# Kernel tuning notes

Hardware: AMD Instinct MI355X
Metric: run time of the kernel (lower is better)

The kernel has to match this reference:

```python
import jax, jax.numpy as jnp
import numpy as np

T = 4096        # tokens
D = 1024        # input_dim
H = 2048        # expert_hidden_dim
O = 1024        # output_dim
E = 8           # num_experts
K = 2           # top_k


def setup_inputs() -> dict:
    key = jax.random.key(0)
    ks = jax.random.split(key, 7)
    s_in = 1.0 / np.sqrt(D)
    s_h = 1.0 / np.sqrt(H)
    return {
        "x": jax.random.normal(ks[0], (T, D), dtype=jnp.float32),
        "Wg": jax.random.uniform(ks[1], (D, E), jnp.float32, -s_in, s_in),
        "bg": jax.random.uniform(ks[2], (E,), jnp.float32, -s_in, s_in),
        "W1": jax.random.uniform(ks[3], (E, D, H), jnp.float32, -s_in, s_in),
        "b1": jax.random.uniform(ks[4], (E, H), jnp.float32, -s_in, s_in),
        "W2": jax.random.uniform(ks[5], (E, H, O), jnp.float32, -s_h, s_h),
        "b2": jax.random.uniform(ks[6], (E, O), jnp.float32, -s_h, s_h),
    }


def reference(x, Wg, bg, W1, b1, W2, b2):
    # Gating: top-k over expert logits, softmax over the k selected logits.
    logits = x @ Wg + bg                                  # [T, E]
    top_vals, top_idx = jax.lax.top_k(logits, K)          # [T, K]
    gates = jax.nn.softmax(top_vals, axis=-1)             # [T, K]

    # Expert MLPs (Linear -> ReLU -> Linear). Each token is processed by the
    # experts it routes to; since an expert's output on x is route-independent,
    # compute all expert outputs once and gather the selected ones (static
    # shapes, jit-friendly equivalent of the masked dispatch loop).
    h = jax.nn.relu(jnp.einsum('td,edh->eth', x, W1) + b1[:, None, :])  # [E,T,H]
    y = jnp.einsum('eth,eho->eto', h, W2) + b2[:, None, :]              # [E,T,O]

    sel = y[top_idx, jnp.arange(T)[:, None]]              # [T, K, O]
    # Weighted combine (scatter_add over batch_idx == per-token sum over K).
    return jnp.sum(sel * gates[..., None], axis=1)        # [T, O]
```

## Files before the change

kernel.cpp:

```cpp
#include <hip/hip_runtime.h>
#include <math.h>


#define T_TOK 4096
#define DIM   1024
#define HID   2048
#define OUTD  1024
#define NE    8

typedef __bf16 bf16_t;
typedef __bf16 bf16x8 __attribute__((ext_vector_type(8)));
typedef float  f32x4  __attribute__((ext_vector_type(4)));

typedef __attribute__((address_space(3))) void       as3_void;
typedef __attribute__((address_space(1))) const void as1_void;
#define GLDS16(src, dst) \
  __builtin_amdgcn_global_load_lds((as1_void*)(src), (as3_void*)(dst), 16, 0, 0)

#define FENCE() asm volatile("" ::: "memory")
#define BARRIER() do { FENCE(); __builtin_amdgcn_s_barrier(); FENCE(); } while (0)

__global__ void k_gate(const float* __restrict__ x, const float* __restrict__ Wg,
                       const float* __restrict__ bg, int* __restrict__ einfo,
                       float2* __restrict__ gpair, bf16_t* __restrict__ xb) {
  int wid  = threadIdx.x >> 6;
  int lane = threadIdx.x & 63;
  int t = blockIdx.x * 4 + wid;

  const float4* xr = (const float4*)(x + (size_t)t * DIM);
  float4 xv4[4];
  float sf[NE];
#pragma unroll
  for (int e = 0; e < NE; ++e) sf[e] = 0.f;

#pragma unroll
  for (int i = 0; i < 4; ++i) {
    int q = lane + 64 * i;
    float4 xv = xr[q];
    xv4[i] = xv;
    int d = q * 4;
#pragma unroll
    for (int c = 0; c < 4; ++c) {
      float xc = (&xv.x)[c];
      const float4* wr = (const float4*)(Wg + (size_t)(d + c) * NE);
      float4 w0 = wr[0], w1 = wr[1];
      sf[0] += xc * w0.x; sf[1] += xc * w0.y;
      sf[2] += xc * w0.z; sf[3] += xc * w0.w;
      sf[4] += xc * w1.x; sf[5] += xc * w1.y;
      sf[6] += xc * w1.z; sf[7] += xc * w1.w;
    }
  }

  ushort4* xbr = (ushort4*)(xb + (size_t)t * DIM);
#pragma unroll
  for (int i = 0; i < 4; ++i) {
    union { bf16_t b[4]; ushort4 u; } cv;
    cv.b[0] = (bf16_t)xv4[i].x; cv.b[1] = (bf16_t)xv4[i].y;
    cv.b[2] = (bf16_t)xv4[i].z; cv.b[3] = (bf16_t)xv4[i].w;
    xbr[lane + 64 * i] = cv.u;
  }

  double s[NE];
#pragma unroll
  for (int e = 0; e < NE; ++e) s[e] = (double)sf[e];
#pragma unroll
  for (int off = 32; off > 0; off >>= 1) {
#pragma unroll
    for (int e = 0; e < NE; ++e) s[e] += __shfl_xor(s[e], off);
  }

  if (lane == 0) {
    double v0 = -1e300, v1 = -1e300;
    int i0 = 0, i1 = 0;
#pragma unroll
    for (int e = 0; e < NE; ++e) {
      double v = s[e] + (double)bg[e];
      if (v > v0)      { v1 = v0; i1 = i0; v0 = v; i0 = e; }
      else if (v > v1) { v1 = v;  i1 = e; }
    }
    float ex = expf((float)(v1 - v0));
    float inv = 1.0f / (1.0f + ex);
    einfo[t] = i0 | (i1 << 8);
    gpair[t] = make_float2(inv, ex * inv);
  }
}

__global__ void k_bin(const int* __restrict__ einfo, const float2* __restrict__ gpair,
                      int* __restrict__ cnt, int* __restrict__ offs,
                      int* __restrict__ elist, float* __restrict__ egate,
                      int* __restrict__ tokrec) {
  __shared__ int scnt[NE];
  int w = threadIdx.x >> 6;
  int lane = threadIdx.x & 63;
  unsigned long long below = (lane == 0) ? 0ull : ((~0ull) >> (64 - lane));
  int base = 0;
  for (int c = 0; c < T_TOK / 64; ++c) {
    int t = c * 64 + lane;
    int ei = einfo[t];
    float2 g = gpair[t];
    int e0 = ei & 0xff, e1 = ei >> 8;
    bool m0 = (e0 == w);
    bool m  = m0 || (e1 == w);
    unsigned long long mask = __ballot(m);
    if (m) {
      int pos = base + (int)__popcll(mask & below);
      elist[w * T_TOK + pos] = t;
      egate[w * T_TOK + pos] = m0 ? g.x : g.y;
      tokrec[2 * t + (m0 ? 0 : 1)] = (w << 16) | pos;
    }
    base += (int)__popcll(mask);
  }
  if (lane == 0) scnt[w] = base;
  __syncthreads();
  if (threadIdx.x == 0) {
    int a = 0;
#pragma unroll
    for (int e = 0; e < NE; ++e) {
      cnt[e] = scnt[e];
      offs[e] = a;
      a += scnt[e];
    }
    offs[NE] = a;
  }
}

__global__ void k_tr(const float* __restrict__ W, bf16_t* __restrict__ Wt,
                     int R, int C) {
  __shared__ float tile[32][33];
  size_t ebase = (size_t)blockIdx.z * R * C;
  int c0 = blockIdx.x * 32, r0 = blockIdx.y * 32;
  int id = threadIdx.x;
  int rc = id >> 5, cc = id & 31;
#pragma unroll
  for (int i = 0; i < 4; ++i)
    tile[rc + i * 8][cc] = W[ebase + (size_t)(r0 + rc + i * 8) * C + c0 + cc];
  __syncthreads();
  int oc = id >> 4, orp = id & 15;
  ushort2* wt2 = (ushort2*)(Wt + ebase);
#pragma unroll
  for (int i = 0; i < 2; ++i) {
    int c = oc + i * 16;
    union { bf16_t b[2]; ushort2 u; } cv;
    cv.b[0] = (bf16_t)tile[orp * 2][c];
    cv.b[1] = (bf16_t)tile[orp * 2 + 1][c];
    wt2[((size_t)(c0 + c) * R + r0 + orp * 2) >> 1] = cv.u;
  }
}

#define STAGE_A(TT, HH) do { \
    char* _d = smem + ((((TT) & 1) * 2 + (HH)) << 14); \
    GLDS16(Abase + offA[HH][0] + (TT) * 128, _d + dstq0 * 16); \
    GLDS16(Abase + offA[HH][1] + (TT) * 128, _d + dstq1 * 16); } while (0)

#define STAGE_B(TT, HH) do { \
    char* _d = smem + 65536 + ((((TT) & 1) * 2 + (HH)) << 14); \
    GLDS16(Bbase + offB[HH][0] + (TT) * 128, _d + dstq0 * 16); \
    GLDS16(Bbase + offB[HH][1] + (TT) * 128, _d + dstq1 * 16); } while (0)

#define PHASE(Q, TT, NTc) do { \
    const char* _a  = smem + ((((TT) & 1) * 2 + ((Q) >> 1)) << 14); \
    const char* _bb = smem + 65536 + ((((TT) & 1) * 2 + ((Q) & 1)) << 14); \
    bf16x8 af[4][2], bfr[2][2]; \
    _Pragma("unroll") for (int i = 0; i < 4; ++i) \
      _Pragma("unroll") for (int kk = 0; kk < 2; ++kk) \
        af[i][kk] = *(const bf16x8*)(_a + rdA[i][kk]); \
    _Pragma("unroll") for (int j = 0; j < 2; ++j) \
      _Pragma("unroll") for (int kk = 0; kk < 2; ++kk) \
        bfr[j][kk] = *(const bf16x8*)(_bb + rdB[j][kk]); \
    if ((Q) == 0)      { if ((TT) + 1 < (NTc)) STAGE_A((TT) + 1, 1); } \
    else if ((Q) == 1) { if ((TT) + 1 < (NTc)) STAGE_B((TT) + 1, 1); } \
    else if ((Q) == 2) { if ((TT) + 2 < (NTc)) STAGE_A((TT) + 2, 0); } \
    else { \
      if ((TT) + 2 < (NTc)) { STAGE_B((TT) + 2, 0); \
        asm volatile("s_waitcnt vmcnt(4)" ::: "memory"); } \
      else { asm volatile("s_waitcnt vmcnt(0)" ::: "memory"); } \
    } \
    BARRIER(); \
    asm volatile("s_waitcnt lgkmcnt(0)" ::: "memory"); \
    __builtin_amdgcn_sched_barrier(0); \
    __builtin_amdgcn_s_setprio(1); \
    _Pragma("unroll") for (int i = 0; i < 4; ++i) \
      _Pragma("unroll") for (int j = 0; j < 2; ++j) \
        _Pragma("unroll") for (int kk = 0; kk < 2; ++kk) \
          acc[((Q) >> 1) * 4 + i][((Q) & 1) * 2 + j] = \
            __builtin_amdgcn_mfma_f32_16x16x32_bf16(af[i][kk], bfr[j][kk], \
                acc[((Q) >> 1) * 4 + i][((Q) & 1) * 2 + j], 0, 0, 0); \
    __builtin_amdgcn_s_setprio(0); \
    BARRIER(); \
  } while (0)

__launch_bounds__(512, 2)
__global__ void k_gemm1(const bf16_t* __restrict__ xb, const bf16_t* __restrict__ W1t,
                        const float* __restrict__ b1, const int* __restrict__ cnt,
                        const int* __restrict__ offs, const int* __restrict__ elist,
                        bf16_t* __restrict__ hbuf) {
  const int e = blockIdx.z;
  const int count = cnt[e];
  const int rt = blockIdx.y;
  if (rt * 256 >= count) return;
  const int nt = blockIdx.x;

  __shared__ __align__(16) char smem[131072];

  const int tid = threadIdx.x, lane = tid & 63, wid = tid >> 6;
  const int wm = wid >> 2, wn = wid & 3;
  const int fr = lane & 15, lh = lane >> 4;

  unsigned offA[2][2], offB[2][2];
  const int dstq0 = tid, dstq1 = 512 + tid;
#pragma unroll
  for (int j = 0; j < 2; ++j) {
    int q = j * 512 + tid;
    int r = q >> 3, sfg = (q & 7) ^ (r & 7);
#pragma unroll
    for (int h = 0; h < 2; ++h) {
      int gr = rt * 256 + h * 128 + r;
      if (gr > count - 1) gr = count - 1;
      int tok = elist[e * T_TOK + gr];
      offA[h][j] = (unsigned)((tok * DIM + sfg * 8) * 2);
      int brow = nt * 256 + h * 128 + r;
      offB[h][j] = (unsigned)(((e * HID + brow) * DIM + sfg * 8) * 2);
    }
  }
  unsigned rdA[4][2], rdB[2][2];
#pragma unroll
  for (int i = 0; i < 4; ++i) {
    int r = wm * 64 + i * 16 + fr;
#pragma unroll
    for (int kk = 0; kk < 2; ++kk)
      rdA[i][kk] = (unsigned)(r * 128 + (((kk * 4 + lh) ^ (r & 7)) * 16));
  }
#pragma unroll
  for (int j = 0; j < 2; ++j) {
    int r = wn * 32 + j * 16 + fr;
#pragma unroll
    for (int kk = 0; kk < 2; ++kk)
      rdB[j][kk] = (unsigned)(r * 128 + (((kk * 4 + lh) ^ (r & 7)) * 16));
  }

  const char* Abase = (const char*)xb;
  const char* Bbase = (const char*)W1t;

  f32x4 acc[8][4];
#pragma unroll
  for (int i = 0; i < 8; ++i)
#pragma unroll
    for (int j = 0; j < 4; ++j) acc[i][j] = (f32x4){0.f, 0.f, 0.f, 0.f};

  const int NT = DIM / 64;
  STAGE_A(0, 0); STAGE_B(0, 0); STAGE_A(0, 1); STAGE_B(0, 1);
  STAGE_A(1, 0); STAGE_B(1, 0);
  asm volatile("s_waitcnt vmcnt(4)" ::: "memory");
  BARRIER();

  for (int t = 0; t < NT; ++t) {
    PHASE(0, t, NT);
    PHASE(1, t, NT);
    PHASE(2, t, NT);
    PHASE(3, t, NT);
  }

  const int hbase = offs[e];
#pragma unroll
  for (int mi = 0; mi < 8; ++mi) {
#pragma unroll
    for (int rr = 0; rr < 4; ++rr) {
      int rowp = rt * 256 + (mi >> 2) * 128 + wm * 64 + (mi & 3) * 16 + lh * 4 + rr;
      if (rowp < count) {
        size_t hrow = (size_t)(hbase + rowp) * HID;
#pragma unroll
        for (int nj = 0; nj < 4; ++nj) {
          int col = nt * 256 + (nj >> 1) * 128 + wn * 32 + (nj & 1) * 16 + fr;
          float v = acc[mi][nj][rr] + b1[e * HID + col];
          hbuf[hrow + col] = (bf16_t)(v > 0.f ? v : 0.f);
        }
      }
    }
  }
}

__launch_bounds__(512, 2)
__global__ void k_gemm2(const bf16_t* __restrict__ hbuf, const bf16_t* __restrict__ W2t,
                        const float* __restrict__ b2, const int* __restrict__ cnt,
                        const int* __restrict__ offs, const float* __restrict__ egate,
                        float* __restrict__ y) {
  const int e = blockIdx.z;
  const int count = cnt[e];
  const int rt = blockIdx.y;
  if (rt * 256 >= count) return;
  const int nt = blockIdx.x;

  __shared__ __align__(16) char smem[131072];

  const int tid = threadIdx.x, lane = tid & 63, wid = tid >> 6;
  const int wm = wid >> 2, wn = wid & 3;
  const int fr = lane & 15, lh = lane >> 4;
  const int hbase = offs[e];

  unsigned offA[2][2], offB[2][2];
  const int dstq0 = tid, dstq1 = 512 + tid;
#pragma unroll
  for (int j = 0; j < 2; ++j) {
    int q = j * 512 + tid;
    int r = q >> 3, sfg = (q & 7) ^ (r & 7);
#pragma unroll
    for (int h = 0; h < 2; ++h) {
      int gr = rt * 256 + h * 128 + r;
      if (gr > count - 1) gr = count - 1;
      offA[h][j] = (unsigned)(((hbase + gr) * HID + sfg * 8) * 2);
      int brow = nt * 256 + h * 128 + r;
      offB[h][j] = (unsigned)(((e * OUTD + brow) * HID + sfg * 8) * 2);
    }
  }
  unsigned rdA[4][2], rdB[2][2];
#pragma unroll
  for (int i = 0; i < 4; ++i) {
    int r = wm * 64 + i * 16 + fr;
#pragma unroll
    for (int kk = 0; kk < 2; ++kk)
      rdA[i][kk] = (unsigned)(r * 128 + (((kk * 4 + lh) ^ (r & 7)) * 16));
  }
#pragma unroll
  for (int j = 0; j < 2; ++j) {
    int r = wn * 32 + j * 16 + fr;
#pragma unroll
    for (int kk = 0; kk < 2; ++kk)
      rdB[j][kk] = (unsigned)(r * 128 + (((kk * 4 + lh) ^ (r & 7)) * 16));
  }

  const char* Abase = (const char*)hbuf;
  const char* Bbase = (const char*)W2t;

  f32x4 acc[8][4];
#pragma unroll
  for (int i = 0; i < 8; ++i)
#pragma unroll
    for (int j = 0; j < 4; ++j) acc[i][j] = (f32x4){0.f, 0.f, 0.f, 0.f};

  const int NT = HID / 64;
  STAGE_A(0, 0); STAGE_B(0, 0); STAGE_A(0, 1); STAGE_B(0, 1);
  STAGE_A(1, 0); STAGE_B(1, 0);
  asm volatile("s_waitcnt vmcnt(4)" ::: "memory");
  BARRIER();

  for (int t = 0; t < NT; ++t) {
    PHASE(0, t, NT);
    PHASE(1, t, NT);
    PHASE(2, t, NT);
    PHASE(3, t, NT);
  }

#pragma unroll
  for (int mi = 0; mi < 8; ++mi) {
#pragma unroll
    for (int rr = 0; rr < 4; ++rr) {
      int rowp = rt * 256 + (mi >> 2) * 128 + wm * 64 + (mi & 3) * 16 + lh * 4 + rr;
      if (rowp < count) {
        float gate = egate[e * T_TOK + rowp];
        size_t yrow = (size_t)(hbase + rowp) * OUTD;
#pragma unroll
        for (int nj = 0; nj < 4; ++nj) {
          int col = nt * 256 + (nj >> 1) * 128 + wn * 32 + (nj & 1) * 16 + fr;
          y[yrow + col] = gate * (acc[mi][nj][rr] + b2[e * OUTD + col]);
        }
      }
    }
  }
}

__global__ void k_combine(const float* __restrict__ y, const int* __restrict__ offs,
                          const int* __restrict__ tokrec, float* __restrict__ out) {
  int t = blockIdx.x;
  int r0 = tokrec[2 * t], r1 = tokrec[2 * t + 1];
  int s0 = offs[r0 >> 16] + (r0 & 0xffff);
  int s1 = offs[r1 >> 16] + (r1 & 0xffff);
  const float4* ya = (const float4*)(y + (size_t)s0 * OUTD);
  const float4* yb = (const float4*)(y + (size_t)s1 * OUTD);
  float4* o = (float4*)(out + (size_t)t * OUTD);
  int i = threadIdx.x;
  float4 a = ya[i], b = yb[i];
  o[i] = make_float4(a.x + b.x, a.y + b.y, a.z + b.z, a.w + b.w);
}

extern "C" void kernel_launch(void* const* d_in, const int* in_sizes, int n_in,
                              void* d_out, int out_size, void* d_ws, size_t ws_size,
                              hipStream_t stream) {
  const float* x  = (const float*)d_in[0];
  const float* Wg = (const float*)d_in[1];
  const float* bg = (const float*)d_in[2];
  const float* W1 = (const float*)d_in[3];
  const float* b1 = (const float*)d_in[4];
  const float* W2 = (const float*)d_in[5];
  const float* b2 = (const float*)d_in[6];
  float* out = (float*)d_out;

  char* ws = (char*)d_ws;
  int*    cnt    = (int*)(ws);
  int*    offs   = (int*)(ws + 1024);
  int*    tokrec = (int*)(ws + 4096);
  int*    einfo  = (int*)(ws + 36864);
  float2* gpair  = (float2*)(ws + 53248);
  int*    elist  = (int*)(ws + 131072);
  float*  egate  = (float*)(ws + 262144);
  bf16_t* W1t    = (bf16_t*)(ws + (1u << 20));
  float*  y      = (float*)(ws + (1u << 20));
  bf16_t* W2t    = (bf16_t*)(ws + (1u << 20) + (32u << 20));
  bf16_t* xb     = (bf16_t*)(ws + (1u << 20) + (64u << 20));
  bf16_t* hbuf   = (bf16_t*)(ws + (1u << 20) + (72u << 20));

  k_gate<<<T_TOK / 4, 256, 0, stream>>>(x, Wg, bg, einfo, gpair, xb);
  k_bin<<<1, 512, 0, stream>>>(einfo, gpair, cnt, offs, elist, egate, tokrec);
  k_tr<<<dim3(HID / 32, DIM / 32, NE), 256, 0, stream>>>(W1, W1t, DIM, HID);
  k_tr<<<dim3(OUTD / 32, HID / 32, NE), 256, 0, stream>>>(W2, W2t, HID, OUTD);

  k_gemm1<<<dim3(HID / 256, 16, NE), 512, 0, stream>>>(
      xb, W1t, b1, cnt, offs, elist, hbuf);
  k_gemm2<<<dim3(OUTD / 256, 16, NE), 512, 0, stream>>>(
      hbuf, W2t, b2, cnt, offs, egate, y);
  k_combine<<<T_TOK, 256, 0, stream>>>(y, offs, tokrec, out);
}
```

Before: 245.7 us.

## Flatten grouped GEMMs over concatenated expert rows with smaller tiles

Both expert GEMMs now use a flat 1D grid over 128-row tiles of the concatenated routed-token rows (8192 rows). A tile that straddles an expert boundary loops over each expert it touches, recomputing the full K loop and writing only the rows in range. This removes the padded per-expert 256-row grid with its early-exit blocks, and shrinks tiles and LDS to raise occupancy. The old deep 4-phase pipeline with s_setprio and explicit vmcnt waits is replaced by a simpler double-buffered loop with a barrier each K step. That may lose latency hiding and adds redundant MFMA work on boundary tiles.

```diff
diff --git a/kernel.cpp b/kernel.cpp
--- a/kernel.cpp
+++ b/kernel.cpp
@@ -16,9 +16,6 @@
 typedef __attribute__((address_space(1))) const void as1_void;
 #define GLDS16(src, dst) \
   __builtin_amdgcn_global_load_lds((as1_void*)(src), (as3_void*)(dst), 16, 0, 0)
-
-#define FENCE() asm volatile("" ::: "memory")
-#define BARRIER() do { FENCE(); __builtin_amdgcn_s_barrier(); FENCE(); } while (0)
 
 __global__ void k_gate(const float* __restrict__ x, const float* __restrict__ Wg,
                        const float* __restrict__ bg, int* __restrict__ einfo,
@@ -147,224 +144,221 @@
   }
 }
 
-#define STAGE_A(TT, HH) do { \
-    char* _d = smem + ((((TT) & 1) * 2 + (HH)) << 14); \
-    GLDS16(Abase + offA[HH][0] + (TT) * 128, _d + dstq0 * 16); \
-    GLDS16(Abase + offA[HH][1] + (TT) * 128, _d + dstq1 * 16); } while (0)
-
-#define STAGE_B(TT, HH) do { \
-    char* _d = smem + 65536 + ((((TT) & 1) * 2 + (HH)) << 14); \
-    GLDS16(Bbase + offB[HH][0] + (TT) * 128, _d + dstq0 * 16); \
-    GLDS16(Bbase + offB[HH][1] + (TT) * 128, _d + dstq1 * 16); } while (0)
-
-#define PHASE(Q, TT, NTc) do { \
-    const char* _a  = smem + ((((TT) & 1) * 2 + ((Q) >> 1)) << 14); \
-    const char* _bb = smem + 65536 + ((((TT) & 1) * 2 + ((Q) & 1)) << 14); \
-    bf16x8 af[4][2], bfr[2][2]; \
-    _Pragma("unroll") for (int i = 0; i < 4; ++i) \
-      _Pragma("unroll") for (int kk = 0; kk < 2; ++kk) \
-        af[i][kk] = *(const bf16x8*)(_a + rdA[i][kk]); \
-    _Pragma("unroll") for (int j = 0; j < 2; ++j) \
-      _Pragma("unroll") for (int kk = 0; kk < 2; ++kk) \
-        bfr[j][kk] = *(const bf16x8*)(_bb + rdB[j][kk]); \
-    if ((Q) == 0)      { if ((TT) + 1 < (NTc)) STAGE_A((TT) + 1, 1); } \
-    else if ((Q) == 1) { if ((TT) + 1 < (NTc)) STAGE_B((TT) + 1, 1); } \
-    else if ((Q) == 2) { if ((TT) + 2 < (NTc)) STAGE_A((TT) + 2, 0); } \
-    else { \
-      if ((TT) + 2 < (NTc)) { STAGE_B((TT) + 2, 0); \
-        asm volatile("s_waitcnt vmcnt(4)" ::: "memory"); } \
-      else { asm volatile("s_waitcnt vmcnt(0)" ::: "memory"); } \
-    } \
-    BARRIER(); \
-    asm volatile("s_waitcnt lgkmcnt(0)" ::: "memory"); \
-    __builtin_amdgcn_sched_barrier(0); \
-    __builtin_amdgcn_s_setprio(1); \
-    _Pragma("unroll") for (int i = 0; i < 4; ++i) \
-      _Pragma("unroll") for (int j = 0; j < 2; ++j) \
-        _Pragma("unroll") for (int kk = 0; kk < 2; ++kk) \
-          acc[((Q) >> 1) * 4 + i][((Q) & 1) * 2 + j] = \
-            __builtin_amdgcn_mfma_f32_16x16x32_bf16(af[i][kk], bfr[j][kk], \
-                acc[((Q) >> 1) * 4 + i][((Q) & 1) * 2 + j], 0, 0, 0); \
-    __builtin_amdgcn_s_setprio(0); \
-    BARRIER(); \
-  } while (0)
-
-__launch_bounds__(512, 2)
+
+__launch_bounds__(512, 4)
 __global__ void k_gemm1(const bf16_t* __restrict__ xb, const bf16_t* __restrict__ W1t,
-                        const float* __restrict__ b1, const int* __restrict__ cnt,
-                        const int* __restrict__ offs, const int* __restrict__ elist,
-                        bf16_t* __restrict__ hbuf) {
-  const int e = blockIdx.z;
-  const int count = cnt[e];
-  const int rt = blockIdx.y;
-  if (rt * 256 >= count) return;
-  const int nt = blockIdx.x;
-
-  __shared__ __align__(16) char smem[131072];
+                        const float* __restrict__ b1, const int* __restrict__ offs,
+                        const int* __restrict__ elist, bf16_t* __restrict__ hbuf) {
+  const int bid = blockIdx.x;
+  const int nt = bid & 7, rt = bid >> 3;
+  const int r0 = rt * 128;
+
+  __shared__ __align__(16) char smem[49152];
 
   const int tid = threadIdx.x, lane = tid & 63, wid = tid >> 6;
   const int wm = wid >> 2, wn = wid & 3;
   const int fr = lane & 15, lh = lane >> 4;
 
-  unsigned offA[2][2], offB[2][2];
-  const int dstq0 = tid, dstq1 = 512 + tid;
-#pragma unroll
-  for (int j = 0; j < 2; ++j) {
-    int q = j * 512 + tid;
-    int r = q >> 3, sfg = (q & 7) ^ (r & 7);
-#pragma unroll
-    for (int h = 0; h < 2; ++h) {
-      int gr = rt * 256 + h * 128 + r;
-      if (gr > count - 1) gr = count - 1;
-      int tok = elist[e * T_TOK + gr];
-      offA[h][j] = (unsigned)((tok * DIM + sfg * 8) * 2);
-      int brow = nt * 256 + h * 128 + r;
-      offB[h][j] = (unsigned)(((e * HID + brow) * DIM + sfg * 8) * 2);
-    }
-  }
-  unsigned rdA[4][2], rdB[2][2];
-#pragma unroll
-  for (int i = 0; i < 4; ++i) {
-    int r = wm * 64 + i * 16 + fr;
-#pragma unroll
-    for (int kk = 0; kk < 2; ++kk)
-      rdA[i][kk] = (unsigned)(r * 128 + (((kk * 4 + lh) ^ (r & 7)) * 16));
-  }
-#pragma unroll
-  for (int j = 0; j < 2; ++j) {
-    int r = wn * 32 + j * 16 + fr;
-#pragma unroll
-    for (int kk = 0; kk < 2; ++kk)
-      rdB[j][kk] = (unsigned)(r * 128 + (((kk * 4 + lh) ^ (r & 7)) * 16));
-  }
-
-  const char* Abase = (const char*)xb;
-  const char* Bbase = (const char*)W1t;
-
-  f32x4 acc[8][4];
-#pragma unroll
-  for (int i = 0; i < 8; ++i)
-#pragma unroll
-    for (int j = 0; j < 4; ++j) acc[i][j] = (f32x4){0.f, 0.f, 0.f, 0.f};
-
-  const int NT = DIM / 64;
-  STAGE_A(0, 0); STAGE_B(0, 0); STAGE_A(0, 1); STAGE_B(0, 1);
-  STAGE_A(1, 0); STAGE_B(1, 0);
-  asm volatile("s_waitcnt vmcnt(4)" ::: "memory");
-  BARRIER();
-
-  for (int t = 0; t < NT; ++t) {
-    PHASE(0, t, NT);
-    PHASE(1, t, NT);
-    PHASE(2, t, NT);
-    PHASE(3, t, NT);
-  }
-
-  const int hbase = offs[e];
-#pragma unroll
-  for (int mi = 0; mi < 8; ++mi) {
-#pragma unroll
-    for (int rr = 0; rr < 4; ++rr) {
-      int rowp = rt * 256 + (mi >> 2) * 128 + wm * 64 + (mi & 3) * 16 + lh * 4 + rr;
-      if (rowp < count) {
-        size_t hrow = (size_t)(hbase + rowp) * HID;
-#pragma unroll
-        for (int nj = 0; nj < 4; ++nj) {
-          int col = nt * 256 + (nj >> 1) * 128 + wn * 32 + (nj & 1) * 16 + fr;
-          float v = acc[mi][nj][rr] + b1[e * HID + col];
-          hbuf[hrow + col] = (bf16_t)(v > 0.f ? v : 0.f);
+  const int ra = tid >> 2, cca = tid & 3;
+  const int ska = cca ^ ((ra >> 1) & 3);
+  const int sA = r0 + ra;
+  int eA = 0;
+  while (offs[eA + 1] <= sA) ++eA;
+  const int tokA = elist[eA * T_TOK + sA - offs[eA]];
+  const char* srcA = (const char*)xb + ((size_t)tokA * DIM + ska * 8) * 2;
+
+  const int rb0 = tid >> 2, ccb0 = tid & 3;
+  const int skb0 = ccb0 ^ ((rb0 >> 1) & 3);
+  const int rb1 = (tid + 512) >> 2, ccb1 = tid & 3;
+  const int skb1 = ccb1 ^ ((rb1 >> 1) & 3);
+
+  unsigned rdA[4], rdB[4];
+#pragma unroll
+  for (int mi = 0; mi < 4; ++mi) {
+    int r = wm * 64 + mi * 16 + fr;
+    rdA[mi] = (unsigned)(r * 64 + ((lh ^ ((r >> 1) & 3)) * 16));
+  }
+#pragma unroll
+  for (int nj = 0; nj < 4; ++nj) {
+    int r = wn * 64 + nj * 16 + fr;
+    rdB[nj] = (unsigned)(r * 64 + ((lh ^ ((r >> 1) & 3)) * 16));
+  }
+
+  const int NT = DIM / 32;
+
+  int e = 0;
+  while (offs[e + 1] <= r0) ++e;
+  for (;;) {
+    const int lo = offs[e] > r0 ? offs[e] : r0;
+    const int hi = offs[e + 1] < r0 + 128 ? offs[e + 1] : r0 + 128;
+
+    const char* srcB0 = (const char*)W1t +
+        ((size_t)(e * HID + nt * 256 + rb0) * DIM + skb0 * 8) * 2;
+    const char* srcB1 = (const char*)W1t +
+        ((size_t)(e * HID + nt * 256 + rb1) * DIM + skb1 * 8) * 2;
+
+    f32x4 acc[4][4];
+#pragma unroll
+    for (int i = 0; i < 4; ++i)
+#pragma unroll
+      for (int j = 0; j < 4; ++j) acc[i][j] = (f32x4){0.f, 0.f, 0.f, 0.f};
+
+    GLDS16(srcA, smem + tid * 16);
+    GLDS16(srcB0, smem + 16384 + tid * 16);
+    GLDS16(srcB1, smem + 16384 + (512 + tid) * 16);
+    __syncthreads();
+
+#pragma unroll 2
+    for (int t = 0; t < NT; ++t) {
+      if (t + 1 < NT) {
+        char* da = smem + ((t + 1) & 1) * 8192;
+        char* db = smem + 16384 + ((t + 1) & 1) * 16384;
+        GLDS16(srcA + (t + 1) * 64, da + tid * 16);
+        GLDS16(srcB0 + (t + 1) * 64, db + tid * 16);
+        GLDS16(srcB1 + (t + 1) * 64, db + (512 + tid) * 16);
+      }
+      const char* a_ = smem + (t & 1) * 8192;
+      const char* b_ = smem + 16384 + (t & 1) * 16384;
+      bf16x8 af[4], bf[4];
+#pragma unroll
+      for (int mi = 0; mi < 4; ++mi) af[mi] = *(const bf16x8*)(a_ + rdA[mi]);
+#pragma unroll
+      for (int nj = 0; nj < 4; ++nj) bf[nj] = *(const bf16x8*)(b_ + rdB[nj]);
+#pragma unroll
+      for (int mi = 0; mi < 4; ++mi)
+#pragma unroll
+        for (int nj = 0; nj < 4; ++nj)
+          acc[mi][nj] = __builtin_amdgcn_mfma_f32_16x16x32_bf16(
+              af[mi], bf[nj], acc[mi][nj], 0, 0, 0);
+      __syncthreads();
+    }
+
+#pragma unroll
+    for (int mi = 0; mi < 4; ++mi) {
+#pragma unroll
+      for (int rr = 0; rr < 4; ++rr) {
+        int row = r0 + wm * 64 + mi * 16 + lh * 4 + rr;
+        if (row >= lo && row < hi) {
+          size_t hrow = (size_t)row * HID;
+#pragma unroll
+          for (int nj = 0; nj < 4; ++nj) {
+            int col = nt * 256 + wn * 64 + nj * 16 + fr;
+            float v = acc[mi][nj][rr] + b1[e * HID + col];
+            hbuf[hrow + col] = (bf16_t)(v > 0.f ? v : 0.f);
+          }
         }
       }
     }
-  }
-}
-
-__launch_bounds__(512, 2)
+
+    if (hi >= r0 + 128) break;
+    ++e;
+  }
+}
+
+__launch_bounds__(256, 4)
 __global__ void k_gemm2(const bf16_t* __restrict__ hbuf, const bf16_t* __restrict__ W2t,
-                        const float* __restrict__ b2, const int* __restrict__ cnt,
-                        const int* __restrict__ offs, const float* __restrict__ egate,
-                        float* __restrict__ y) {
-  const int e = blockIdx.z;
-  const int count = cnt[e];
-  const int rt = blockIdx.y;
-  if (rt * 256 >= count) return;
-  const int nt = blockIdx.x;
-
-  __shared__ __align__(16) char smem[131072];
+                        const float* __restrict__ b2, const int* __restrict__ offs,
+                        const float* __restrict__ egate, float* __restrict__ y) {
+  const int bid = blockIdx.x;
+  const int nt = bid & 7, rt = bid >> 3;
+  const int r0 = rt * 128;
+
+  __shared__ __align__(16) char smem[32768];
 
   const int tid = threadIdx.x, lane = tid & 63, wid = tid >> 6;
-  const int wm = wid >> 2, wn = wid & 3;
+  const int wm = wid >> 1, wn = wid & 1;
   const int fr = lane & 15, lh = lane >> 4;
-  const int hbase = offs[e];
-
-  unsigned offA[2][2], offB[2][2];
-  const int dstq0 = tid, dstq1 = 512 + tid;
-#pragma unroll
-  for (int j = 0; j < 2; ++j) {
-    int q = j * 512 + tid;
-    int r = q >> 3, sfg = (q & 7) ^ (r & 7);
-#pragma unroll
-    for (int h = 0; h < 2; ++h) {
-      int gr = rt * 256 + h * 128 + r;
-      if (gr > count - 1) gr = count - 1;
-      offA[h][j] = (unsigned)(((hbase + gr) * HID + sfg * 8) * 2);
-      int brow = nt * 256 + h * 128 + r;
-      offB[h][j] = (unsigned)(((e * OUTD + brow) * HID + sfg * 8) * 2);
-    }
-  }
-  unsigned rdA[4][2], rdB[2][2];
-#pragma unroll
-  for (int i = 0; i < 4; ++i) {
-    int r = wm * 64 + i * 16 + fr;
-#pragma unroll
-    for (int kk = 0; kk < 2; ++kk)
-      rdA[i][kk] = (unsigned)(r * 128 + (((kk * 4 + lh) ^ (r & 7)) * 16));
-  }
-#pragma unroll
-  for (int j = 0; j < 2; ++j) {
-    int r = wn * 32 + j * 16 + fr;
-#pragma unroll
-    for (int kk = 0; kk < 2; ++kk)
-      rdB[j][kk] = (unsigned)(r * 128 + (((kk * 4 + lh) ^ (r & 7)) * 16));
-  }
-
-  const char* Abase = (const char*)hbuf;
-  const char* Bbase = (const char*)W2t;
-
-  f32x4 acc[8][4];
-#pragma unroll
-  for (int i = 0; i < 8; ++i)
-#pragma unroll
-    for (int j = 0; j < 4; ++j) acc[i][j] = (f32x4){0.f, 0.f, 0.f, 0.f};
-
-  const int NT = HID / 64;
-  STAGE_A(0, 0); STAGE_B(0, 0); STAGE_A(0, 1); STAGE_B(0, 1);
-  STAGE_A(1, 0); STAGE_B(1, 0);
-  asm volatile("s_waitcnt vmcnt(4)" ::: "memory");
-  BARRIER();
-
-  for (int t = 0; t < NT; ++t) {
-    PHASE(0, t, NT);
-    PHASE(1, t, NT);
-    PHASE(2, t, NT);
-    PHASE(3, t, NT);
-  }
-
-#pragma unroll
-  for (int mi = 0; mi < 8; ++mi) {
-#pragma unroll
-    for (int rr = 0; rr < 4; ++rr) {
-      int rowp = rt * 256 + (mi >> 2) * 128 + wm * 64 + (mi & 3) * 16 + lh * 4 + rr;
-      if (rowp < count) {
-        float gate = egate[e * T_TOK + rowp];
-        size_t yrow = (size_t)(hbase + rowp) * OUTD;
-#pragma unroll
-        for (int nj = 0; nj < 4; ++nj) {
-          int col = nt * 256 + (nj >> 1) * 128 + wn * 32 + (nj & 1) * 16 + fr;
-          y[yrow + col] = gate * (acc[mi][nj][rr] + b2[e * OUTD + col]);
+
+  const int ra0 = tid >> 2,          ska0 = (tid & 3) ^ ((ra0 >> 1) & 3);
+  const int ra1 = (tid + 256) >> 2,  ska1 = (tid & 3) ^ ((ra1 >> 1) & 3);
+  const char* srcA0 = (const char*)hbuf + ((size_t)(r0 + ra0) * HID + ska0 * 8) * 2;
+  const char* srcA1 = (const char*)hbuf + ((size_t)(r0 + ra1) * HID + ska1 * 8) * 2;
+
+  const int rb0 = tid >> 2,          skb0 = (tid & 3) ^ ((rb0 >> 1) & 3);
+  const int rb1 = (tid + 256) >> 2,  skb1 = (tid & 3) ^ ((rb1 >> 1) & 3);
+
+  unsigned rdA[4], rdB[4];
+#pragma unroll
+  for (int mi = 0; mi < 4; ++mi) {
+    int r = wm * 64 + mi * 16 + fr;
+    rdA[mi] = (unsigned)(r * 64 + ((lh ^ ((r >> 1) & 3)) * 16));
+  }
+#pragma unroll
+  for (int nj = 0; nj < 4; ++nj) {
+    int r = wn * 64 + nj * 16 + fr;
+    rdB[nj] = (unsigned)(r * 64 + ((lh ^ ((r >> 1) & 3)) * 16));
+  }
+
+  const int NT = HID / 32;
+
+  int e = 0;
+  while (offs[e + 1] <= r0) ++e;
+  for (;;) {
+    const int lo = offs[e] > r0 ? offs[e] : r0;
+    const int hi = offs[e + 1] < r0 + 128 ? offs[e + 1] : r0 + 128;
+
+    const char* srcB0 = (const char*)W2t +
+        ((size_t)(e * OUTD + nt * 128 + rb0) * HID + skb0 * 8) * 2;
+    const char* srcB1 = (const char*)W2t +
+        ((size_t)(e * OUTD + nt * 128 + rb1) * HID + skb1 * 8) * 2;
+
+    f32x4 acc[4][4];
+#pragma unroll
+    for (int i = 0; i < 4; ++i)
+#pragma unroll
+      for (int j = 0; j < 4; ++j) acc[i][j] = (f32x4){0.f, 0.f, 0.f, 0.f};
+
+    GLDS16(srcA0, smem + tid * 16);
+    GLDS16(srcA1, smem + (256 + tid) * 16);
+    GLDS16(srcB0, smem + 16384 + tid * 16);
+    GLDS16(srcB1, smem + 16384 + (256 + tid) * 16);
+    __syncthreads();
+
+#pragma unroll 2
+    for (int t = 0; t < NT; ++t) {
+      if (t + 1 < NT) {
+        char* da = smem + ((t + 1) & 1) * 8192;
+        char* db = smem + 16384 + ((t + 1) & 1) * 8192;
+        GLDS16(srcA0 + (t + 1) * 64, da + tid * 16);
+        GLDS16(srcA1 + (t + 1) * 64, da + (256 + tid) * 16);
+        GLDS16(srcB0 + (t + 1) * 64, db + tid * 16);
+        GLDS16(srcB1 + (t + 1) * 64, db + (256 + tid) * 16);
+      }
+      const char* a_ = smem + (t & 1) * 8192;
+      const char* b_ = smem + 16384 + (t & 1) * 8192;
+      bf16x8 af[4], bf[4];
+#pragma unroll
+      for (int mi = 0; mi < 4; ++mi) af[mi] = *(const bf16x8*)(a_ + rdA[mi]);
+#pragma unroll
+      for (int nj = 0; nj < 4; ++nj) bf[nj] = *(const bf16x8*)(b_ + rdB[nj]);
+#pragma unroll
+      for (int mi = 0; mi < 4; ++mi)
+#pragma unroll
+        for (int nj = 0; nj < 4; ++nj)
+          acc[mi][nj] = __builtin_amdgcn_mfma_f32_16x16x32_bf16(
+              af[mi], bf[nj], acc[mi][nj], 0, 0, 0);
+      __syncthreads();
+    }
+
+#pragma unroll
+    for (int mi = 0; mi < 4; ++mi) {
+#pragma unroll
+      for (int rr = 0; rr < 4; ++rr) {
+        int row = r0 + wm * 64 + mi * 16 + lh * 4 + rr;
+        if (row >= lo && row < hi) {
+          float gate = egate[e * T_TOK + row - offs[e]];
+          size_t yrow = (size_t)row * OUTD;
+#pragma unroll
+          for (int nj = 0; nj < 4; ++nj) {
+            int col = nt * 128 + wn * 64 + nj * 16 + fr;
+            y[yrow + col] = gate * (acc[mi][nj][rr] + b2[e * OUTD + col]);
+          }
         }
       }
     }
+
+    if (hi >= r0 + 128) break;
+    ++e;
   }
 }
 
@@ -413,9 +407,7 @@
   k_tr<<<dim3(HID / 32, DIM / 32, NE), 256, 0, stream>>>(W1, W1t, DIM, HID);
   k_tr<<<dim3(OUTD / 32, HID / 32, NE), 256, 0, stream>>>(W2, W2t, HID, OUTD);
 
-  k_gemm1<<<dim3(HID / 256, 16, NE), 512, 0, stream>>>(
-      xb, W1t, b1, cnt, offs, elist, hbuf);
-  k_gemm2<<<dim3(OUTD / 256, 16, NE), 512, 0, stream>>>(
-      hbuf, W2t, b2, cnt, offs, egate, y);
+  k_gemm1<<<512, 512, 0, stream>>>(xb, W1t, b1, offs, elist, hbuf);
+  k_gemm2<<<512, 256, 0, stream>>>(hbuf, W2t, b2, offs, egate, y);
   k_combine<<<T_TOK, 256, 0, stream>>>(y, offs, tokrec, out);
 }
```

Measured after the change: 304.1 us. 1.24x slower.
